# Kernel optimization log

Measured on AMD Instinct MI355X. Metric: run time of the kernel, lower is better.

## Reference

```python
import math
import jax, jax.numpy as jnp
import numpy as np

NUM_HEADS = 4
HEAD_DIM = 384


def reshape_fortran(x, shape):
    # column-major (Fortran) reshape, matching the torch reverse-permute trick
    x = jnp.transpose(x, tuple(reversed(range(x.ndim))))
    x = x.reshape(tuple(reversed(shape)))
    return jnp.transpose(x, tuple(reversed(range(len(shape)))))


def rel_pos_rotate(data):
    # data: [b, n_heads, L=2M-1, S] -> [b, n_heads, S, S]
    data = jnp.transpose(data, (0, 2, 3, 1))  # [b, d0=L, d1=S, d2=H]
    b, d0, d1, d2 = data.shape
    data = jnp.concatenate([data, jnp.zeros((b, d1, d1, d2), data.dtype)], axis=1)
    data = reshape_fortran(data, (b, (d0 + d1) * d1, 1, d2))
    data = data[:, :(d1 + d0 - 1) * d1]
    data = reshape_fortran(data, (b, d0 + d1 - 1, d1, d2))
    n = d0 // 2
    data = jnp.swapaxes(data[:, n:n + d1], 1, 2)  # [b, d1, d1, d2]
    return jnp.transpose(data, (0, 3, 1, 2))      # [b, H, S, S]


def setup_inputs() -> dict:
    key = jax.random.key(0)
    ks = jax.random.split(key, 5)
    B, S, D = 4, 920, 1536
    M = 920
    return {
        "hidden_states": jax.random.normal(ks[0], (B, S, D), jnp.float32),
        "q_w": jax.random.normal(ks[1], (D, NUM_HEADS * HEAD_DIM), jnp.float32) * 0.02,
        "k_w": jax.random.normal(ks[2], (D, NUM_HEADS * HEAD_DIM), jnp.float32) * 0.02,
        "v_w": jax.random.normal(ks[3], (D, NUM_HEADS * HEAD_DIM), jnp.float32) * 0.02,
        "dist_emb": jax.random.normal(ks[4], (2 * M - 1, HEAD_DIM), jnp.float32) * 0.02,
    }


def reference(hidden_states, q_w, k_w, v_w, dist_emb):
    B, S, D = hidden_states.shape

    def heads(x):  # [B,S,H*hd] -> [B,H,S,hd]
        return jnp.transpose(x.reshape(B, S, NUM_HEADS, HEAD_DIM), (0, 2, 1, 3))

    # query is pre-scaled by 1/sqrt(head_dim), matching the torch code
    q = heads((hidden_states @ q_w) / math.sqrt(HEAD_DIM))
    k = heads(hidden_states @ k_w)
    v = heads(hidden_states @ v_w)

    scores = jnp.einsum("bhqd,bhkd->bhqk", q, k)  # [B,H,S,S]
    # relative position scores: [B,H,L,S] then skew-rotated into [B,H,S,S]
    rel = jnp.einsum("ld,bhsd->bhls", dist_emb, q)
    scores = scores + rel_pos_rotate(rel)

    probs = jax.nn.softmax(scores, axis=-1)
    ctx = jnp.einsum("bhqk,bhkd->bhqd", probs, v)  # [B,H,S,hd]
    ctx = jnp.transpose(ctx, (0, 2, 1, 3)).reshape(B, S, NUM_HEADS * HEAD_DIM)
    return ctx
```

## Files before the change

kernel.cpp:

```cpp
#include <hip/hip_runtime.h>
#include <cstdint>
#include <cstddef>

#define SEQ   920
#define DM    1536
#define DH    384
#define NHD   4
#define NB    4
#define NBH   16
#define MTOK  3680
#define NREL  1839

typedef short          bf16x8 __attribute__((ext_vector_type(8)));
typedef float          f32x4  __attribute__((ext_vector_type(4)));
typedef unsigned short u16x4  __attribute__((ext_vector_type(4)));

__device__ __forceinline__ unsigned short f2bf(float f){
  union{float f; unsigned u;} v; v.f = f;
  unsigned r = v.u + 0x7FFFu + ((v.u >> 16) & 1u);
  return (unsigned short)(r >> 16);
}
__device__ __forceinline__ float bf2f(unsigned short h){
  union{unsigned u; float f;} v; v.u = ((unsigned)h) << 16;
  return v.f;
}
__device__ __forceinline__ f32x4 mfma_bf16(bf16x8 a, bf16x8 b, f32x4 c){
  return __builtin_amdgcn_mfma_f32_16x16x32_bf16(a, b, c, 0, 0, 0);
}
__device__ __forceinline__ void gload_lds16(const void* g, void* l){
  __builtin_amdgcn_global_load_lds((const __attribute__((address_space(1))) void*)g,
                                   (__attribute__((address_space(3))) void*)l, 16, 0, 0);
}

__global__ __launch_bounds__(256) void k_f2bf(const float* __restrict__ src,
                                              unsigned short* __restrict__ dst, int n){
  int i = (blockIdx.x * 256 + threadIdx.x) * 4;
  int stride = gridDim.x * 256 * 4;
  for(; i + 3 < n; i += stride){
    f32x4 v = *(const f32x4*)(src + i);
    u16x4 o; o.x = f2bf(v.x); o.y = f2bf(v.y); o.z = f2bf(v.z); o.w = f2bf(v.w);
    *(u16x4*)(dst + i) = o;
  }
}

__global__ __launch_bounds__(256) void k_wt3(const float* __restrict__ qw,
                                             const float* __restrict__ kw,
                                             const float* __restrict__ vw,
                                             unsigned short* __restrict__ wt){
  __shared__ float t[32][33];
  const float* w = blockIdx.z == 0 ? qw : (blockIdx.z == 1 ? kw : vw);
  int k0 = blockIdx.x * 32, n0 = blockIdx.y * 32;
  int tx = threadIdx.x, ty = threadIdx.y;
  #pragma unroll
  for(int j = 0; j < 4; j++)
    t[ty*4+j][tx] = w[(size_t)(k0 + ty*4 + j) * DM + n0 + tx];
  __syncthreads();
  #pragma unroll
  for(int j = 0; j < 4; j++)
    wt[(size_t)(blockIdx.z*DM + n0 + ty*4 + j) * DM + k0 + tx] = f2bf(t[tx][ty*4+j]);
}

template<class Epi>
__device__ __forceinline__ void gemm192(const unsigned short* __restrict__ A, int lda, int Amax,
                                        const unsigned short* __restrict__ B, int ldb, int Bmax,
                                        int K, int m0, int n0, Epi epi){
  __shared__ unsigned short As[3*192*64];
  __shared__ unsigned short Bs[3*192*64];
  const int tid = threadIdx.x;
  const int w = tid >> 6, l = tid & 63;
  const int lg = l >> 4, lo = l & 15;
  const int wm = w >> 2, wn = w & 3;

  const char* ga[3]; const char* gb[3];
  #pragma unroll
  for(int r = 0; r < 3; r++){
    int row = r*64 + (tid >> 3);
    int gslot = (tid & 7) ^ (row & 7);
    int ar = m0 + row; ar = ar < Amax ? ar : Amax - 1;
    ga[r] = (const char*)A + (size_t)ar*lda*2 + gslot*16;
    int br = n0 + row; br = br < Bmax ? br : Bmax - 1;
    gb[r] = (const char*)B + (size_t)br*ldb*2 + gslot*16;
  }
  const int ldst = tid * 16;

  auto stage = [&](int kt, int slot){
    size_t koff = (size_t)kt * 128;
    #pragma unroll
    for(int r = 0; r < 3; r++){
      gload_lds16(ga[r] + koff, (char*)As + slot*24576 + r*8192 + ldst);
      gload_lds16(gb[r] + koff, (char*)Bs + slot*24576 + r*8192 + ldst);
    }
  };

  f32x4 acc[6][3] = {};
  const int sw = (lo & 7) << 4;

  auto compute = [&](int slot){
    const char* Ab = (const char*)As + slot*24576;
    const char* Bb = (const char*)Bs + slot*24576;
    bf16x8 af[6][2], bf[3][2];
    #pragma unroll
    for(int fi = 0; fi < 6; fi++){
      int row = wm*96 + fi*16 + lo;
      #pragma unroll
      for(int kk = 0; kk < 2; kk++)
        af[fi][kk] = *(const bf16x8*)(Ab + row*128 + ((kk*64 + lg*16) ^ sw));
    }
    #pragma unroll
    for(int fj = 0; fj < 3; fj++){
      int row = wn*48 + fj*16 + lo;
      #pragma unroll
      for(int kk = 0; kk < 2; kk++)
        bf[fj][kk] = *(const bf16x8*)(Bb + row*128 + ((kk*64 + lg*16) ^ sw));
    }
    __builtin_amdgcn_s_setprio(1);
    #pragma unroll
    for(int kk = 0; kk < 2; kk++)
      #pragma unroll
      for(int fi = 0; fi < 6; fi++)
        #pragma unroll
        for(int fj = 0; fj < 3; fj++)
          acc[fi][fj] = mfma_bf16(af[fi][kk], bf[fj][kk], acc[fi][fj]);
    __builtin_amdgcn_s_setprio(0);
  };

  const int nk = K >> 6;
  stage(0, 0);
  stage(1, 1);
  int st = 0;
  for(int t = 0; t < nk; t++){
    if(t + 2 < nk){
      int s2 = st + 2 >= 3 ? st - 1 : st + 2;
      stage(t + 2, s2);
      asm volatile("s_waitcnt vmcnt(12)" ::: "memory");
    } else if(t + 1 < nk){
      asm volatile("s_waitcnt vmcnt(6)" ::: "memory");
    } else {
      asm volatile("s_waitcnt vmcnt(0)" ::: "memory");
    }
    __builtin_amdgcn_s_barrier();
    compute(st);
    __builtin_amdgcn_s_barrier();
    st = st + 1 >= 3 ? 0 : st + 1;
  }

  #pragma unroll
  for(int fi = 0; fi < 6; fi++)
    #pragma unroll
    for(int fj = 0; fj < 3; fj++){
      int m = m0 + wm*96 + fi*16 + lg*4;
      int n = n0 + wn*48 + fj*16 + lo;
      epi(m, n, acc[fi][fj]);
    }
}

__global__ __launch_bounds__(512) void k_proj(const unsigned short* __restrict__ X,
                                              const unsigned short* __restrict__ Wt,
                                              unsigned short* __restrict__ Qb,
                                              unsigned short* __restrict__ Kb,
                                              unsigned short* __restrict__ Vt){
  int bid = blockIdx.x;
  int wg  = (bid & 7) * 60 + (bid >> 3);
  int m0 = (wg % 20) * 192, n0 = (wg / 20) * 192;
  gemm192(X, DM, MTOK, Wt, DM, 3*DM, DM, m0, n0,
    [=] __device__ (int m, int n, f32x4 v4){
      if(m >= MTOK) return;
      int which = n / DM, r = n % DM, h = r / DH, d = r % DH;
      int b = m / SEQ, s = m % SEQ;
      int bh = b * NHD + h;
      if(which == 2){
        u16x4 o;
        o.x = f2bf(v4.x); o.y = f2bf(v4.y); o.z = f2bf(v4.z); o.w = f2bf(v4.w);
        *(u16x4*)(Vt + ((size_t)bh*DH + d)*SEQ + s) = o;
      } else if(which == 0){
        #pragma unroll
        for(int i = 0; i < 4; i++)
          Qb[((size_t)bh*SEQ + s + i)*DH + d] = f2bf(v4[i] * 0.05103103630798287f);
      } else {
        #pragma unroll
        for(int i = 0; i < 4; i++)
          Kb[((size_t)bh*SEQ + s + i)*DH + d] = f2bf(v4[i]);
      }
    });
}

__global__ __launch_bounds__(512) void k_rel(const unsigned short* __restrict__ Qb,
                                             const unsigned short* __restrict__ E,
                                             unsigned short* __restrict__ relS){
  int m0 = blockIdx.x * 192, n0 = blockIdx.y * 192;
  int s0 = m0 % SEQ;
  int qlo = s0, qhi = s0 + 191;
  if(qhi >= SEQ){ qlo = 0; qhi = SEQ - 1; }
  if(n0 + 191 < 919 - qhi || n0 > 1838 - qlo) return;
  gemm192(Qb, DH, NBH*SEQ, E, DH, NREL, DH, m0, n0,
    [=] __device__ (int m, int n, f32x4 v4){
      #pragma unroll
      for(int i = 0; i < 4; i++){
        int mi = m + i;
        if(mi >= NBH*SEQ) continue;
        int q = mi % SEQ;
        int j = n - 919 + q;
        if(j < 0 || j >= SEQ) continue;
        relS[(size_t)mi*SEQ + j] = f2bf(v4[i]);
      }
    });
}

__global__ __launch_bounds__(256) void k_attn(const unsigned short* __restrict__ Qb,
                                              const unsigned short* __restrict__ Kb,
                                              const unsigned short* __restrict__ Vt,
                                              const unsigned short* __restrict__ relS,
                                              float* __restrict__ out){
  __shared__ unsigned short Ks[32*384];
  __shared__ unsigned short Vs[384*32];
  __shared__ unsigned short Pl[32*40];
  __shared__ float sums[2][32];
  const int bh = blockIdx.y, qt = blockIdx.x, q0 = qt * 32;
  const int tid = threadIdx.x, w = tid >> 6, l = tid & 63;
  const int mi = w >> 1, ni = w & 1;
  const int lg = l >> 4, lo = l & 15;

  int qrow = q0 + mi*16 + lo; if(qrow > SEQ-1) qrow = SEQ-1;
  const char* Qrow = (const char*)(Qb + ((size_t)bh*SEQ + qrow)*DH);
  bf16x8 qf[12];
  #pragma unroll
  for(int ks = 0; ks < 12; ks++) qf[ks] = *(const bf16x8*)(Qrow + ks*64 + lg*16);

  f32x4 ctx[2][6] = {};
  float ps[4] = {0.f, 0.f, 0.f, 0.f};

  for(int kt = 0; kt < 29; kt++){
    const int k0 = kt * 32;
    __syncthreads();
    #pragma unroll
    for(int r = 0; r < 6; r++){
      int o = r*4096 + w*1024 + l*16;
      int row = o / 768, c = o - row*768;
      int csw = c ^ ((row & 7) << 4);
      int krow = k0 + row; if(krow > SEQ-1) krow = SEQ-1;
      gload_lds16((const char*)Kb + ((size_t)bh*SEQ + krow)*768 + csw, (char*)Ks + o);
      int d = o >> 6, c2 = o & 63;
      int vcol = k0*2 + c2; if(vcol > 1824) vcol = 1824;
      gload_lds16((const char*)Vt + ((size_t)bh*DH + d)*1840 + vcol, (char*)Vs + o);
    }
    __syncthreads();
    f32x4 accs = {};
    const int krowB = ni*16 + lo;
    const char* KsB = (const char*)Ks + krowB*768;
    const int sw = (krowB & 7) << 4;
    #pragma unroll
    for(int ks = 0; ks < 12; ks++){
      bf16x8 bf = *(const bf16x8*)(KsB + ((ks*64 + lg*16) ^ sw));
      accs = mfma_bf16(qf[ks], bf, accs);
    }
    unsigned short ph[4];
    #pragma unroll
    for(int i = 0; i < 4; i++){
      int q = q0 + mi*16 + lg*4 + i; if(q > SEQ-1) q = SEQ-1;
      int k = k0 + ni*16 + lo;
      int kc = k > SEQ-1 ? SEQ-1 : k;
      float rl = bf2f(relS[((size_t)bh*SEQ + q)*SEQ + kc]);
      float p = __expf(accs[i] + rl);
      if(k >= SEQ) p = 0.f;
      ps[i] += p;
      ph[i] = f2bf(p);
    }
    #pragma unroll
    for(int i = 0; i < 4; i++)
      *(unsigned short*)((char*)Pl + (mi*16 + lg*4 + i)*80 + (ni*16 + lo)*2) = ph[i];
    __syncthreads();
    bf16x8 pa0 = *(const bf16x8*)((char*)Pl + lo*80 + lg*16);
    bf16x8 pa1 = *(const bf16x8*)((char*)Pl + (16 + lo)*80 + lg*16);
    #pragma unroll
    for(int nj = 0; nj < 6; nj++){
      int d = w*96 + nj*16 + lo;
      bf16x8 vb = *(const bf16x8*)((char*)Vs + d*64 + lg*16);
      ctx[0][nj] = mfma_bf16(pa0, vb, ctx[0][nj]);
      ctx[1][nj] = mfma_bf16(pa1, vb, ctx[1][nj]);
    }
  }
  #pragma unroll
  for(int i = 0; i < 4; i++){
    float v = ps[i];
    v += __shfl_xor(v, 1); v += __shfl_xor(v, 2);
    v += __shfl_xor(v, 4); v += __shfl_xor(v, 8);
    if(lo == 0) sums[ni][mi*16 + lg*4 + i] = v;
  }
  __syncthreads();
  const int b = bh >> 2, h = bh & 3;
  #pragma unroll
  for(int m2 = 0; m2 < 2; m2++){
    #pragma unroll
    for(int i = 0; i < 4; i++){
      int ql = m2*16 + lg*4 + i;
      int q = q0 + ql;
      if(q >= SEQ) continue;
      float inv = 1.0f / (sums[0][ql] + sums[1][ql]);
      #pragma unroll
      for(int nj = 0; nj < 6; nj++){
        int d = w*96 + nj*16 + lo;
        out[((size_t)(b*SEQ + q))*DM + h*DH + d] = ctx[m2][nj][i] * inv;
      }
    }
  }
}

extern "C" void kernel_launch(void* const* d_in, const int* in_sizes, int n_in,
                              void* d_out, int out_size, void* d_ws, size_t ws_size,
                              hipStream_t stream){
  const float* X  = (const float*)d_in[0];
  const float* qw = (const float*)d_in[1];
  const float* kw = (const float*)d_in[2];
  const float* vw = (const float*)d_in[3];
  const float* de = (const float*)d_in[4];
  float* out = (float*)d_out;
  char* ws = (char*)d_ws;

  unsigned short* Qb   = (unsigned short*)ws;
  unsigned short* Kb   = (unsigned short*)(ws + 11304960);
  unsigned short* Vt   = (unsigned short*)(ws + 22609920);
  unsigned short* Eb   = (unsigned short*)(ws + 33914880);
  char* regionR        = ws + 35327232;
  unsigned short* relS = (unsigned short*)regionR;
  unsigned short* Xb   = (unsigned short*)regionR;
  unsigned short* Wt   = (unsigned short*)(regionR + 11304960);

  k_f2bf<<<dim3(2048), dim3(256), 0, stream>>>(X,  Xb, MTOK*DM);
  k_f2bf<<<dim3(690),  dim3(256), 0, stream>>>(de, Eb, NREL*DH);
  k_wt3<<<dim3(48,48,3), dim3(32,8), 0, stream>>>(qw, kw, vw, Wt);
  k_proj<<<dim3(480), dim3(512), 0, stream>>>(Xb, Wt, Qb, Kb, Vt);
  k_rel<<<dim3(77,10), dim3(512), 0, stream>>>(Qb, Eb, relS);
  k_attn<<<dim3(29,16), dim3(256), 0, stream>>>(Qb, Kb, Vt, relS, out);
}
```

Measured before the change: 212.3 us.

## Read K and V directly from global memory in attention kernel, use 64-key tiles

The attention kernel no longer stages K and V tiles into shared memory with async LDS loads. Each wave now reads its K rows and V slices straight from global memory (relying on cache), and the key tile grows from 32 to 64, which halves the loop iterations and barriers. This cuts LDS usage, which may raise occupancy, and removes the load-then-sync phase. In exchange it risks redundant global/L2 traffic, since the waves in a block now each fetch the same K and V data, and uncoalesced row-strided reads.

```diff
diff --git a/kernel.cpp b/kernel.cpp
--- a/kernel.cpp
+++ b/kernel.cpp
@@ -211,11 +211,9 @@
                                               const unsigned short* __restrict__ Vt,
                                               const unsigned short* __restrict__ relS,
                                               float* __restrict__ out){
-  __shared__ unsigned short Ks[32*384];
-  __shared__ unsigned short Vs[384*32];
-  __shared__ unsigned short Pl[32*40];
+  __shared__ unsigned short Pl[32*72];
   __shared__ float sums[2][32];
-  const int bh = blockIdx.y, qt = blockIdx.x, q0 = qt * 32;
+  const int bh = blockIdx.y, q0 = blockIdx.x * 32;
   const int tid = threadIdx.x, w = tid >> 6, l = tid & 63;
   const int mi = w >> 1, ni = w & 1;
   const int lg = l >> 4, lo = l & 15;
@@ -226,58 +224,60 @@
   #pragma unroll
   for(int ks = 0; ks < 12; ks++) qf[ks] = *(const bf16x8*)(Qrow + ks*64 + lg*16);
 
+  const char* Kbh = (const char*)(Kb + (size_t)bh*SEQ*DH);
+  const char* Vbh = (const char*)(Vt + (size_t)bh*DH*SEQ);
+  const unsigned short* Rbh = relS + (size_t)bh*SEQ*SEQ;
+
   f32x4 ctx[2][6] = {};
   float ps[4] = {0.f, 0.f, 0.f, 0.f};
 
-  for(int kt = 0; kt < 29; kt++){
-    const int k0 = kt * 32;
+  for(int kt = 0; kt < 15; kt++){
+    const int k0 = kt * 64;
+    f32x4 sacc[2] = {};
+    #pragma unroll
+    for(int f = 0; f < 2; f++){
+      int krow = k0 + ni*32 + f*16 + lo; if(krow > SEQ-1) krow = SEQ-1;
+      const char* Kr = Kbh + (size_t)krow*768;
+      #pragma unroll
+      for(int ks = 0; ks < 12; ks++){
+        bf16x8 kb = *(const bf16x8*)(Kr + ks*64 + lg*16);
+        sacc[f] = mfma_bf16(qf[ks], kb, sacc[f]);
+      }
+    }
+    #pragma unroll
+    for(int f = 0; f < 2; f++){
+      #pragma unroll
+      for(int i = 0; i < 4; i++){
+        int q = q0 + mi*16 + lg*4 + i; if(q > SEQ-1) q = SEQ-1;
+        int k = k0 + ni*32 + f*16 + lo;
+        int kc = k > SEQ-1 ? SEQ-1 : k;
+        float rl = bf2f(Rbh[(size_t)q*SEQ + kc]);
+        float p = __expf(sacc[f][i] + rl);
+        if(k >= SEQ) p = 0.f;
+        ps[i] += p;
+        *(unsigned short*)((char*)Pl + (mi*16 + lg*4 + i)*144 + (ni*32 + f*16 + lo)*2) = f2bf(p);
+      }
+    }
     __syncthreads();
-    #pragma unroll
-    for(int r = 0; r < 6; r++){
-      int o = r*4096 + w*1024 + l*16;
-      int row = o / 768, c = o - row*768;
-      int csw = c ^ ((row & 7) << 4);
-      int krow = k0 + row; if(krow > SEQ-1) krow = SEQ-1;
-      gload_lds16((const char*)Kb + ((size_t)bh*SEQ + krow)*768 + csw, (char*)Ks + o);
-      int d = o >> 6, c2 = o & 63;
-      int vcol = k0*2 + c2; if(vcol > 1824) vcol = 1824;
-      gload_lds16((const char*)Vt + ((size_t)bh*DH + d)*1840 + vcol, (char*)Vs + o);
-    }
-    __syncthreads();
-    f32x4 accs = {};
-    const int krowB = ni*16 + lo;
-    const char* KsB = (const char*)Ks + krowB*768;
-    const int sw = (krowB & 7) << 4;
-    #pragma unroll
-    for(int ks = 0; ks < 12; ks++){
-      bf16x8 bf = *(const bf16x8*)(KsB + ((ks*64 + lg*16) ^ sw));
-      accs = mfma_bf16(qf[ks], bf, accs);
-    }
-    unsigned short ph[4];
-    #pragma unroll
-    for(int i = 0; i < 4; i++){
-      int q = q0 + mi*16 + lg*4 + i; if(q > SEQ-1) q = SEQ-1;
-      int k = k0 + ni*16 + lo;
-      int kc = k > SEQ-1 ? SEQ-1 : k;
-      float rl = bf2f(relS[((size_t)bh*SEQ + q)*SEQ + kc]);
-      float p = __expf(accs[i] + rl);
-      if(k >= SEQ) p = 0.f;
-      ps[i] += p;
-      ph[i] = f2bf(p);
-    }
-    #pragma unroll
-    for(int i = 0; i < 4; i++)
-      *(unsigned short*)((char*)Pl + (mi*16 + lg*4 + i)*80 + (ni*16 + lo)*2) = ph[i];
-    __syncthreads();
-    bf16x8 pa0 = *(const bf16x8*)((char*)Pl + lo*80 + lg*16);
-    bf16x8 pa1 = *(const bf16x8*)((char*)Pl + (16 + lo)*80 + lg*16);
+    bf16x8 pa[2][2];
+    #pragma unroll
+    for(int m2 = 0; m2 < 2; m2++)
+      #pragma unroll
+      for(int ksl = 0; ksl < 2; ksl++)
+        pa[m2][ksl] = *(const bf16x8*)((char*)Pl + (m2*16 + lo)*144 + ksl*64 + lg*16);
     #pragma unroll
     for(int nj = 0; nj < 6; nj++){
       int d = w*96 + nj*16 + lo;
-      bf16x8 vb = *(const bf16x8*)((char*)Vs + d*64 + lg*16);
-      ctx[0][nj] = mfma_bf16(pa0, vb, ctx[0][nj]);
-      ctx[1][nj] = mfma_bf16(pa1, vb, ctx[1][nj]);
-    }
+      const char* Vr = Vbh + (size_t)d*1840;
+      #pragma unroll
+      for(int ksl = 0; ksl < 2; ksl++){
+        int ob = k0*2 + ksl*64 + lg*16; if(ob > 1824) ob = 1824;
+        bf16x8 vb = *(const bf16x8*)(Vr + ob);
+        ctx[0][nj] = mfma_bf16(pa[0][ksl], vb, ctx[0][nj]);
+        ctx[1][nj] = mfma_bf16(pa[1][ksl], vb, ctx[1][nj]);
+      }
+    }
+    __syncthreads();
   }
   #pragma unroll
   for(int i = 0; i < 4; i++){
```

Measured after the change: 256.7 us. 20.9% more time.
